# Kernel optimization log

Measured on AMD Instinct MI355X. Metric: run time of the kernel, lower is better.

The kernel has to match this reference:

```python
import jax, jax.numpy as jnp
import numpy as np

N, E, D, C, H = 50000, 800000, 128, 64, 2
NEG_SLOPE = 0.2


def gat_layer(x, src, dst, W, a_src, a_dst, b, heads, concat):
    # PyG GATConv (eval mode: attention dropout disabled), add_self_loops already in src/dst.
    n = x.shape[0]
    c = W.shape[1] // heads
    xl = (x @ W).reshape(n, heads, c)                      # [N,H,C]
    s = jnp.einsum('nhc,hc->nh', xl, a_src)                # alpha_src per node
    d = jnp.einsum('nhc,hc->nh', xl, a_dst)                # alpha_dst per node
    e = jax.nn.leaky_relu(s[src] + d[dst], NEG_SLOPE)      # [E,H]
    emax = jax.lax.stop_gradient(jax.ops.segment_max(e, dst, num_segments=n))
    ex = jnp.exp(e - emax[dst])
    denom = jax.ops.segment_sum(ex, dst, num_segments=n)   # every node has a self-loop -> denom > 0
    alpha = ex / denom[dst]                                # softmax over incoming edges
    msg = xl[src] * alpha[:, :, None]                      # [E,H,C]
    out = jax.ops.segment_sum(msg, dst, num_segments=n)    # [N,H,C]
    out = out.reshape(n, heads * c) if concat else out.mean(axis=1)
    return out + b


def setup_inputs() -> dict:
    key = jax.random.key(0)
    ks = jax.random.split(key, 16)
    x = jax.random.normal(ks[0], (N, D), dtype=jnp.float32)
    edge_index = jax.random.randint(ks[1], (2, E), 0, N, dtype=jnp.int64)
    def glorot(k, shape):
        fan = shape[0] + shape[-1]
        return jax.random.normal(k, shape, dtype=jnp.float32) * np.sqrt(2.0 / fan).astype(np.float32)
    # layer 0: D -> H*C (concat)
    W0 = glorot(ks[2], (D, H * C)); att_src0 = glorot(ks[3], (H, C)); att_dst0 = glorot(ks[4], (H, C)); b0 = jnp.zeros((H * C,), jnp.float32)
    # layer 1: H*C -> H*C (concat)
    W1 = glorot(ks[5], (H * C, H * C)); att_src1 = glorot(ks[6], (H, C)); att_dst1 = glorot(ks[7], (H, C)); b1 = jnp.zeros((H * C,), jnp.float32)
    # layer 2: H*C -> C (heads=1, concat=False)
    W2 = glorot(ks[8], (H * C, C)); att_src2 = glorot(ks[9], (1, C)); att_dst2 = glorot(ks[10], (1, C)); b2 = jnp.zeros((C,), jnp.float32)
    return dict(x=x, edge_index=edge_index,
                W0=W0, att_src0=att_src0, att_dst0=att_dst0, b0=b0,
                W1=W1, att_src1=att_src1, att_dst1=att_dst1, b1=b1,
                W2=W2, att_src2=att_src2, att_dst2=att_dst2, b2=b2)


def reference(x, edge_index, W0, att_src0, att_dst0, b0, W1, att_src1, att_dst1, b1, W2, att_src2, att_dst2, b2):
    n = x.shape[0]
    loops = jnp.arange(n, dtype=edge_index.dtype)
    src = jnp.concatenate([edge_index[0], loops])
    dst = jnp.concatenate([edge_index[1], loops])
    h = gat_layer(x, src, dst, W0, att_src0, att_dst0, b0, H, True)
    h = jax.nn.elu(h)
    h = gat_layer(h, src, dst, W1, att_src1, att_dst1, b1, H, True)
    h = jax.nn.elu(h)
    h = gat_layer(h, src, dst, W2, att_src2, att_dst2, b2, 1, False)
    return h
```

## Files before the change

### kernel.cpp

```cpp
#include <hip/hip_runtime.h>
#include <hip/hip_fp16.h>
#include <math.h>

#define NEG_SLOPE 0.2f

__device__ __forceinline__ float lrelu(float v) { return v > 0.0f ? v : NEG_SLOPE * v; }

typedef _Float16 half8 __attribute__((ext_vector_type(8)));
typedef float floatx4 __attribute__((ext_vector_type(4)));


__global__ __launch_bounds__(256) void count_win_k(const int* __restrict__ dst,
                                                   int* __restrict__ counts,
                                                   int e, int winSize) {
  const int win = blockIdx.x & 7;
  const int lo = win * winSize;
  const int hi = lo + winSize;
  const int base = (blockIdx.x >> 3) * 4096 + threadIdx.x;
  for (int t = 0; t < 16; ++t) {
    int i = base + t * 256;
    if (i < e) {
      int d = dst[i];
      if (d >= lo && d < hi) atomicAdd(&counts[d], 1);
    }
  }
}

__global__ __launch_bounds__(256) void block_sum_k(const int* __restrict__ counts,
                                                   int* __restrict__ blockSums, int n) {
  int i = blockIdx.x * 256 + threadIdx.x;
  int v = (i < n) ? counts[i] : 0;
  for (int o = 32; o > 0; o >>= 1) v += __shfl_xor(v, o);
  __shared__ int ws[4];
  if ((threadIdx.x & 63) == 0) ws[threadIdx.x >> 6] = v;
  __syncthreads();
  if (threadIdx.x == 0) blockSums[blockIdx.x] = ws[0] + ws[1] + ws[2] + ws[3];
}

__global__ __launch_bounds__(256) void scan_sums_k(int* __restrict__ blockSums, int nb,
                                                   int* __restrict__ total_out) {
  __shared__ int sh[256];
  const int tid = threadIdx.x;
  int run = 0;
  for (int base = 0; base < nb; base += 256) {
    int i = base + tid;
    int v = (i < nb) ? blockSums[i] : 0;
    sh[tid] = v;
    __syncthreads();
    for (int o = 1; o < 256; o <<= 1) {
      int t = (tid >= o) ? sh[tid - o] : 0;
      __syncthreads();
      sh[tid] += t;
      __syncthreads();
    }
    int chunkTotal = sh[255];
    if (i < nb) blockSums[i] = run + sh[tid] - v;
    __syncthreads();
    run += chunkTotal;
  }
  if (tid == 0) *total_out = run;
}

__global__ __launch_bounds__(256) void scan_apply_k(int* __restrict__ counts_cursor,
                                                    const int* __restrict__ blockOffs,
                                                    int* __restrict__ row_ptr, int n) {
  __shared__ int sh[256];
  const int tid = threadIdx.x;
  const int i = blockIdx.x * 256 + tid;
  int v = (i < n) ? counts_cursor[i] : 0;
  sh[tid] = v;
  __syncthreads();
  for (int o = 1; o < 256; o <<= 1) {
    int t = (tid >= o) ? sh[tid - o] : 0;
    __syncthreads();
    sh[tid] += t;
    __syncthreads();
  }
  if (i < n) {
    int excl = blockOffs[blockIdx.x] + sh[tid] - v;
    row_ptr[i] = excl;
    counts_cursor[i] = excl;
  }
}

__global__ __launch_bounds__(256) void scatter_win_k(const int* __restrict__ src,
                                                     const int* __restrict__ dst,
                                                     int* __restrict__ cursor,
                                                     int* __restrict__ csr,
                                                     int e, int winSize) {
  const int win = blockIdx.x & 7;
  const int lo = win * winSize;
  const int hi = lo + winSize;
  const int base = (blockIdx.x >> 3) * 4096 + threadIdx.x;
  for (int t = 0; t < 16; ++t) {
    int i = base + t * 256;
    if (i < e) {
      int d = dst[i];
      if (d >= lo && d < hi) {
        int pos = atomicAdd(&cursor[d], 1);
        csr[pos] = src[i];
      }
    }
  }
}


__global__ __launch_bounds__(256) void cvt_wt3_k(const float* __restrict__ W0,
                                                 const float* __restrict__ W1,
                                                 const float* __restrict__ W2,
                                                 __half* __restrict__ Wt0,
                                                 __half* __restrict__ Wt1,
                                                 __half* __restrict__ Wt2) {
  int i = blockIdx.x * 256 + threadIdx.x;
  if (i < 128 * 128) {
    int col = i >> 7, k = i & 127;
    Wt0[i] = __float2half(W0[k * 128 + col]);
    Wt1[i] = __float2half(W1[k * 128 + col]);
    if (col < 64) Wt2[(size_t)col * 128 + k] = __float2half(W2[k * 64 + col]);
  }
}


template<int M, int H_, bool IN_F32>
__global__ __launch_bounds__(256) void gemm_attn_mfma_k(const void* __restrict__ Xin,
                                                        const __half* __restrict__ Wt,
                                                        const float* __restrict__ a_src,
                                                        const float* __restrict__ a_dst,
                                                        __half* __restrict__ Yh,
                                                        float* __restrict__ sArr,
                                                        float* __restrict__ dArr, int n) {
  constexpr int CT = M / 16;
  constexpr int LP = 136;
  __shared__ _Float16 Xs[64 * LP];
  __shared__ _Float16 Ws[M * LP];
  const int tid = threadIdx.x;
  const int w = tid >> 6;
  const int lane = tid & 63;
  const int l15 = lane & 15;
  const int quad = lane >> 4;
  const int rb = blockIdx.x * 64;

  if (IN_F32) {
    const float* Xf = (const float*)Xin;
    for (int t = 0; t < 8; ++t) {
      int idx = tid + t * 256;
      int r = idx >> 5, c4 = idx & 31;
      float4 v = make_float4(0.f, 0.f, 0.f, 0.f);
      if (rb + r < n) v = *(const float4*)(Xf + (size_t)(rb + r) * 128 + c4 * 4);
      __half2 a = __floats2half2_rn(v.x, v.y);
      __half2 b = __floats2half2_rn(v.z, v.w);
      uint2 pk;
      pk.x = *(unsigned int*)&a;
      pk.y = *(unsigned int*)&b;
      *(uint2*)&Xs[r * LP + c4 * 4] = pk;
    }
  } else {
    const __half* Xh = (const __half*)Xin;
    for (int t = 0; t < 4; ++t) {
      int idx = tid + t * 256;
      int r = idx >> 4, c8 = idx & 15;
      uint4 v = make_uint4(0, 0, 0, 0);
      if (rb + r < n) v = *(const uint4*)(Xh + (size_t)(rb + r) * 128 + c8 * 8);
      *(uint4*)&Xs[r * LP + c8 * 8] = v;
    }
  }
  for (int t = 0; t < CT; ++t) {
    int idx = tid + t * 256;
    int r = idx >> 4, c8 = idx & 15;
    *(uint4*)&Ws[r * LP + c8 * 8] = *(const uint4*)(Wt + (size_t)r * 128 + c8 * 8);
  }
  __syncthreads();

  floatx4 acc[CT];
  for (int c = 0; c < CT; ++c)
    for (int j = 0; j < 4; ++j) acc[c][j] = 0.f;

  const int arow = w * 16 + l15;
  for (int kq = 0; kq < 4; ++kq) {
    half8 a = *(const half8*)&Xs[arow * LP + kq * 32 + quad * 8];
    for (int c = 0; c < CT; ++c) {
      half8 b = *(const half8*)&Ws[(c * 16 + l15) * LP + kq * 32 + quad * 8];
      acc[c] = __builtin_amdgcn_mfma_f32_16x16x32_f16(a, b, acc[c], 0, 0, 0);
    }
  }

  float as[CT], ad[CT];
  for (int c = 0; c < CT; ++c) {
    as[c] = a_src[c * 16 + l15];
    ad[c] = a_dst[c * 16 + l15];
  }

  for (int c = 0; c < CT; ++c) {
    for (int r = 0; r < 4; ++r) {
      int row = rb + w * 16 + quad * 4 + r;
      if (row < n) Yh[(size_t)row * M + c * 16 + l15] = __float2half(acc[c][r]);
    }
  }

  for (int r = 0; r < 4; ++r) {
    int row = rb + w * 16 + quad * 4 + r;
    float s0 = 0.f, d0 = 0.f, s1 = 0.f, d1 = 0.f;
    if (H_ == 2) {
      for (int c = 0; c < CT / 2; ++c) {
        s0 += acc[c][r] * as[c];
        d0 += acc[c][r] * ad[c];
      }
      for (int c = CT / 2; c < CT; ++c) {
        s1 += acc[c][r] * as[c];
        d1 += acc[c][r] * ad[c];
      }
    } else {
      for (int c = 0; c < CT; ++c) {
        s0 += acc[c][r] * as[c];
        d0 += acc[c][r] * ad[c];
      }
    }
    for (int o = 1; o < 16; o <<= 1) {
      s0 += __shfl_xor(s0, o);
      d0 += __shfl_xor(d0, o);
      if (H_ == 2) {
        s1 += __shfl_xor(s1, o);
        d1 += __shfl_xor(d1, o);
      }
    }
    if (l15 == 0 && row < n) {
      if (H_ == 2) {
        sArr[row * 2] = s0;
        sArr[row * 2 + 1] = s1;
        dArr[row * 2] = d0;
        dArr[row * 2 + 1] = d1;
      } else {
        sArr[row] = s0;
        dArr[row] = d0;
      }
    }
  }
}


#define IDX_CAP 1024

__global__ __launch_bounds__(256) void edge2h_k(const __half* __restrict__ xlh,
                                                const float* __restrict__ sArr,
                                                const float* __restrict__ dArr,
                                                const float* __restrict__ bias,
                                                const int* __restrict__ row_ptr,
                                                const int* __restrict__ csr,
                                                __half* __restrict__ outh, int n) {
  const int tid = threadIdx.x;
  const int wid = tid >> 6;
  const int lane = tid & 63;
  const int sub = lane >> 4;
  const int l16 = lane & 15;
  const int nodeBase = blockIdx.x * 16;

  __shared__ int rp[17];
  __shared__ int idxS[IDX_CAP];
  if (tid < 17) {
    int nn = nodeBase + tid;
    rp[tid] = row_ptr[nn < n ? nn : n];
  }
  __syncthreads();
  const int rowBeg = rp[0];
  int lim = rp[16] - rowBeg;
  if (lim > IDX_CAP) lim = IDX_CAP;
  for (int i = tid; i < lim; i += 256) idxS[i] = csr[rowBeg + i];
  __syncthreads();

  const int li = (wid << 2) + sub;
  const int node = nodeBase + li;
  if (node >= n) return;
  const int row = rp[li];
  const int deg = rp[li + 1] - row;
  const int head = l16 >> 3;
  const uint4* __restrict__ xq = (const uint4*)xlh;
  const float dnsel = dArr[node * 2 + head];

  float svS = sArr[node * 2 + head];
  uint4 pS = xq[(size_t)node * 16 + l16];

  float a0 = 0.f, a1 = 0.f, a2 = 0.f, a3 = 0.f;
  float a4 = 0.f, a5 = 0.f, a6 = 0.f, a7 = 0.f;
  float den = 0.f;

  auto body = [&](const int* __restrict__ ip) {
    int j = 0;
    for (; j + 4 <= deg; j += 4) {
      int idx[4];
      float sv[4];
      uint4 p[4];
#pragma unroll
      for (int t = 0; t < 4; ++t) idx[t] = ip[j + t];
#pragma unroll
      for (int t = 0; t < 4; ++t) sv[t] = sArr[idx[t] * 2 + head];
#pragma unroll
      for (int t = 0; t < 4; ++t) p[t] = xq[(size_t)idx[t] * 16 + l16];
#pragma unroll
      for (int t = 0; t < 4; ++t) {
        float w = __expf(lrelu(sv[t] + dnsel));
        den += w;
        float2 v0 = __half22float2(*(__half2*)&p[t].x);
        float2 v1 = __half22float2(*(__half2*)&p[t].y);
        float2 v2 = __half22float2(*(__half2*)&p[t].z);
        float2 v3 = __half22float2(*(__half2*)&p[t].w);
        a0 += w * v0.x; a1 += w * v0.y; a2 += w * v1.x; a3 += w * v1.y;
        a4 += w * v2.x; a5 += w * v2.y; a6 += w * v3.x; a7 += w * v3.y;
      }
    }
    for (; j < deg; ++j) {
      int i0 = ip[j];
      float sv = sArr[i0 * 2 + head];
      uint4 p = xq[(size_t)i0 * 16 + l16];
      float w = __expf(lrelu(sv + dnsel));
      den += w;
      float2 v0 = __half22float2(*(__half2*)&p.x);
      float2 v1 = __half22float2(*(__half2*)&p.y);
      float2 v2 = __half22float2(*(__half2*)&p.z);
      float2 v3 = __half22float2(*(__half2*)&p.w);
      a0 += w * v0.x; a1 += w * v0.y; a2 += w * v1.x; a3 += w * v1.y;
      a4 += w * v2.x; a5 += w * v2.y; a6 += w * v3.x; a7 += w * v3.y;
    }
  };
  if (row - rowBeg + deg <= IDX_CAP) body(idxS + (row - rowBeg));
  else body(csr + row);

  float wS = __expf(lrelu(svS + dnsel));
  den += wS;
  {
    float2 v0 = __half22float2(*(__half2*)&pS.x);
    float2 v1 = __half22float2(*(__half2*)&pS.y);
    float2 v2 = __half22float2(*(__half2*)&pS.z);
    float2 v3 = __half22float2(*(__half2*)&pS.w);
    a0 += wS * v0.x; a1 += wS * v0.y; a2 += wS * v1.x; a3 += wS * v1.y;
    a4 += wS * v2.x; a5 += wS * v2.y; a6 += wS * v3.x; a7 += wS * v3.y;
  }

  float wi = 1.f / den;
  float4 bbA = ((const float4*)bias)[l16 * 2];
  float4 bbB = ((const float4*)bias)[l16 * 2 + 1];
  float r0 = a0 * wi + bbA.x;
  float r1 = a1 * wi + bbA.y;
  float r2 = a2 * wi + bbA.z;
  float r3 = a3 * wi + bbA.w;
  float r4 = a4 * wi + bbB.x;
  float r5 = a5 * wi + bbB.y;
  float r6 = a6 * wi + bbB.z;
  float r7 = a7 * wi + bbB.w;
  r0 = r0 > 0.f ? r0 : expm1f(r0);
  r1 = r1 > 0.f ? r1 : expm1f(r1);
  r2 = r2 > 0.f ? r2 : expm1f(r2);
  r3 = r3 > 0.f ? r3 : expm1f(r3);
  r4 = r4 > 0.f ? r4 : expm1f(r4);
  r5 = r5 > 0.f ? r5 : expm1f(r5);
  r6 = r6 > 0.f ? r6 : expm1f(r6);
  r7 = r7 > 0.f ? r7 : expm1f(r7);
  __half2 h0 = __floats2half2_rn(r0, r1);
  __half2 h1 = __floats2half2_rn(r2, r3);
  __half2 h2 = __floats2half2_rn(r4, r5);
  __half2 h3 = __floats2half2_rn(r6, r7);
  uint4 pk;
  pk.x = *(unsigned int*)&h0;
  pk.y = *(unsigned int*)&h1;
  pk.z = *(unsigned int*)&h2;
  pk.w = *(unsigned int*)&h3;
  ((uint4*)outh)[(size_t)node * 16 + l16] = pk;
}

__global__ __launch_bounds__(256) void edge1h_k(const __half* __restrict__ xlh,
                                                const float* __restrict__ sArr,
                                                const float* __restrict__ dArr,
                                                const float* __restrict__ bias,
                                                const int* __restrict__ row_ptr,
                                                const int* __restrict__ csr,
                                                float* __restrict__ outp, int n) {
  const int tid = threadIdx.x;
  const int wid = tid >> 6;
  const int lane = tid & 63;
  const int sub = lane >> 4;
  const int l16 = lane & 15;
  const int nodeBase = blockIdx.x * 16;

  __shared__ int rp[17];
  __shared__ int idxS[IDX_CAP];
  if (tid < 17) {
    int nn = nodeBase + tid;
    rp[tid] = row_ptr[nn < n ? nn : n];
  }
  __syncthreads();
  const int rowBeg = rp[0];
  int lim = rp[16] - rowBeg;
  if (lim > IDX_CAP) lim = IDX_CAP;
  for (int i = tid; i < lim; i += 256) idxS[i] = csr[rowBeg + i];
  __syncthreads();

  const int li = (wid << 2) + sub;
  const int node = nodeBase + li;
  if (node >= n) return;
  const int row = rp[li];
  const int deg = rp[li + 1] - row;
  const uint2* __restrict__ xq = (const uint2*)xlh;
  const float dn = dArr[node];

  float svS = sArr[node];
  uint2 pS = xq[(size_t)node * 16 + l16];

  float a0 = 0.f, a1 = 0.f, a2 = 0.f, a3 = 0.f;
  float den = 0.f;

  auto body = [&](const int* __restrict__ ip) {
    int j = 0;
    for (; j + 4 <= deg; j += 4) {
      int idx[4];
      float sv[4];
      uint2 p[4];
#pragma unroll
      for (int t = 0; t < 4; ++t) idx[t] = ip[j + t];
#pragma unroll
      for (int t = 0; t < 4; ++t) sv[t] = sArr[idx[t]];
#pragma unroll
      for (int t = 0; t < 4; ++t) p[t] = xq[(size_t)idx[t] * 16 + l16];
#pragma unroll
      for (int t = 0; t < 4; ++t) {
        float w = __expf(lrelu(sv[t] + dn));
        den += w;
        float2 v0 = __half22float2(*(__half2*)&p[t].x);
        float2 v1 = __half22float2(*(__half2*)&p[t].y);
        a0 += w * v0.x; a1 += w * v0.y; a2 += w * v1.x; a3 += w * v1.y;
      }
    }
    for (; j < deg; ++j) {
      int i0 = ip[j];
      float sv = sArr[i0];
      uint2 p = xq[(size_t)i0 * 16 + l16];
      float w = __expf(lrelu(sv + dn));
      den += w;
      float2 v0 = __half22float2(*(__half2*)&p.x);
      float2 v1 = __half22float2(*(__half2*)&p.y);
      a0 += w * v0.x; a1 += w * v0.y; a2 += w * v1.x; a3 += w * v1.y;
    }
  };
  if (row - rowBeg + deg <= IDX_CAP) body(idxS + (row - rowBeg));
  else body(csr + row);

  float wS = __expf(lrelu(svS + dn));
  den += wS;
  {
    float2 v0 = __half22float2(*(__half2*)&pS.x);
    float2 v1 = __half22float2(*(__half2*)&pS.y);
    a0 += wS * v0.x; a1 += wS * v0.y; a2 += wS * v1.x; a3 += wS * v1.y;
  }

  float wi = 1.f / den;
  float4 bb = ((const float4*)bias)[l16];
  float4 r;
  r.x = a0 * wi + bb.x;
  r.y = a1 * wi + bb.y;
  r.z = a2 * wi + bb.z;
  r.w = a3 * wi + bb.w;
  ((float4*)outp)[(size_t)node * 16 + l16] = r;
}


extern "C" void kernel_launch(void* const* d_in, const int* in_sizes, int n_in,
                              void* d_out, int out_size, void* d_ws, size_t ws_size,
                              hipStream_t stream) {
  const float* x  = (const float*)d_in[0];
  const int* ei   = (const int*)d_in[1];
  const float* W0 = (const float*)d_in[2];
  const float* as0 = (const float*)d_in[3];
  const float* ad0 = (const float*)d_in[4];
  const float* b0 = (const float*)d_in[5];
  const float* W1 = (const float*)d_in[6];
  const float* as1 = (const float*)d_in[7];
  const float* ad1 = (const float*)d_in[8];
  const float* b1 = (const float*)d_in[9];
  const float* W2 = (const float*)d_in[10];
  const float* as2 = (const float*)d_in[11];
  const float* ad2 = (const float*)d_in[12];
  const float* b2 = (const float*)d_in[13];
  float* out = (float*)d_out;

  const int n = in_sizes[0] / 128;
  const int e = in_sizes[1] / 2;
  const int* srcIdx = ei;
  const int* dstIdx = ei + e;

  float* ws = (float*)d_ws;
  float* sArr = ws;
  float* dArr = sArr + (size_t)n * 2;
  __half* xlh = (__half*)(dArr + (size_t)n * 2);
  __half* bufHh = xlh + (size_t)n * 128;
  __half* Wt0 = bufHh + (size_t)n * 128;
  __half* Wt1 = Wt0 + 128 * 128;
  __half* Wt2 = Wt1 + 128 * 128;
  int* csr = (int*)(Wt2 + 64 * 128);
  int* row_ptr = csr + e;
  int* cursor = row_ptr + (n + 1);
  int* blockSums = cursor + n;

  const int nb = (n + 255) / 256;
  const int winSize = (n + 7) / 8;
  const int gwin = 8 * ((e + 4095) / 4096);

  cvt_wt3_k<<<(128 * 128 + 255) / 256, 256, 0, stream>>>(W0, W1, W2, Wt0, Wt1, Wt2);

  hipMemsetAsync(cursor, 0, (size_t)n * sizeof(int), stream);
  count_win_k<<<gwin, 256, 0, stream>>>(dstIdx, cursor, e, winSize);
  block_sum_k<<<nb, 256, 0, stream>>>(cursor, blockSums, n);
  scan_sums_k<<<1, 256, 0, stream>>>(blockSums, nb, row_ptr + n);
  scan_apply_k<<<nb, 256, 0, stream>>>(cursor, blockSums, row_ptr, n);
  scatter_win_k<<<gwin, 256, 0, stream>>>(srcIdx, dstIdx, cursor, csr, e, winSize);

  const int gb = (n + 63) / 64;
  const int gq = (n + 15) / 16;

  gemm_attn_mfma_k<128, 2, true><<<gb, 256, 0, stream>>>(x, Wt0, as0, ad0, xlh, sArr, dArr, n);
  edge2h_k<<<gq, 256, 0, stream>>>(xlh, sArr, dArr, b0, row_ptr, csr, bufHh, n);

  gemm_attn_mfma_k<128, 2, false><<<gb, 256, 0, stream>>>(bufHh, Wt1, as1, ad1, xlh, sArr, dArr, n);
  edge2h_k<<<gq, 256, 0, stream>>>(xlh, sArr, dArr, b1, row_ptr, csr, bufHh, n);

  gemm_attn_mfma_k<64, 1, false><<<gb, 256, 0, stream>>>(bufHh, Wt2, as2, ad2, xlh, sArr, dArr, n);
  edge1h_k<<<gq, 256, 0, stream>>>(xlh, sArr, dArr, b2, row_ptr, csr, out, n);
}
```

Baseline: 302.0 us.

## Fuse CSR count and prefix scan into one kernel with grid-wide spin barriers

```diff
diff --git a/kernel.cpp b/kernel.cpp
--- a/kernel.cpp
+++ b/kernel.cpp
@@ -3,6 +3,7 @@
 #include <math.h>
 
 #define NEG_SLOPE 0.2f
+#define IDX_CAP 1024
 
 __device__ __forceinline__ float lrelu(float v) { return v > 0.0f ? v : NEG_SLOPE * v; }
 
@@ -10,64 +11,65 @@
 typedef float floatx4 __attribute__((ext_vector_type(4)));
 
 
-__global__ __launch_bounds__(256) void count_win_k(const int* __restrict__ dst,
-                                                   int* __restrict__ counts,
-                                                   int e, int winSize) {
-  const int win = blockIdx.x & 7;
-  const int lo = win * winSize;
-  const int hi = lo + winSize;
-  const int base = (blockIdx.x >> 3) * 4096 + threadIdx.x;
-  for (int t = 0; t < 16; ++t) {
-    int i = base + t * 256;
-    if (i < e) {
-      int d = dst[i];
-      if (d >= lo && d < hi) atomicAdd(&counts[d], 1);
-    }
-  }
-}
-
-__global__ __launch_bounds__(256) void block_sum_k(const int* __restrict__ counts,
-                                                   int* __restrict__ blockSums, int n) {
-  int i = blockIdx.x * 256 + threadIdx.x;
-  int v = (i < n) ? counts[i] : 0;
-  for (int o = 32; o > 0; o >>= 1) v += __shfl_xor(v, o);
-  __shared__ int ws[4];
-  if ((threadIdx.x & 63) == 0) ws[threadIdx.x >> 6] = v;
-  __syncthreads();
-  if (threadIdx.x == 0) blockSums[blockIdx.x] = ws[0] + ws[1] + ws[2] + ws[3];
-}
-
-__global__ __launch_bounds__(256) void scan_sums_k(int* __restrict__ blockSums, int nb,
-                                                   int* __restrict__ total_out) {
+__global__ __launch_bounds__(256) void cvt_wt3_zero_k(const float* __restrict__ W0,
+                                                      const float* __restrict__ W1,
+                                                      const float* __restrict__ W2,
+                                                      __half* __restrict__ Wt0,
+                                                      __half* __restrict__ Wt1,
+                                                      __half* __restrict__ Wt2,
+                                                      int* __restrict__ cursor,
+                                                      int* __restrict__ ctl, int n) {
+  const int i = blockIdx.x * 256 + threadIdx.x;
+  const int stride = gridDim.x * 256;
+  for (int k = i; k < n; k += stride) cursor[k] = 0;
+  if (blockIdx.x == 0 && threadIdx.x < 4) ctl[threadIdx.x] = 0;
+  if (i < 128 * 128) {
+    int col = i >> 7, k = i & 127;
+    Wt0[i] = __float2half(W0[k * 128 + col]);
+    Wt1[i] = __float2half(W1[k * 128 + col]);
+    if (col < 64) Wt2[(size_t)col * 128 + k] = __float2half(W2[k * 64 + col]);
+  }
+}
+
+
+__global__ __launch_bounds__(256) void count_scan_k(const int* __restrict__ dst,
+                                                    int* __restrict__ cursor,
+                                                    int* __restrict__ row_ptr,
+                                                    int* __restrict__ blockSums,
+                                                    int* __restrict__ ctl,
+                                                    int n, int e, int winSize, int nbc) {
+  const int tid = threadIdx.x;
+
+  {
+    const int win = blockIdx.x & 7;
+    const int lo = win * winSize;
+    const int hi = lo + winSize;
+    const int base = (blockIdx.x >> 3) * 4096 + tid;
+    for (int t = 0; t < 16; ++t) {
+      int i = base + t * 256;
+      if (i < e) {
+        int d = dst[i];
+        if (d >= lo && d < hi) atomicAdd(&cursor[d], 1);
+      }
+    }
+  }
+  __threadfence();
+  if (tid == 0)
+    __hip_atomic_fetch_add(&ctl[0], 1, __ATOMIC_ACQ_REL, __HIP_MEMORY_SCOPE_AGENT);
+  if (blockIdx.x >= nbc) return;
+
+  if (tid == 0) {
+    while (__hip_atomic_load(&ctl[0], __ATOMIC_ACQUIRE, __HIP_MEMORY_SCOPE_AGENT) <
+           (int)gridDim.x)
+      __builtin_amdgcn_s_sleep(2);
+  }
+  __syncthreads();
+
   __shared__ int sh[256];
-  const int tid = threadIdx.x;
-  int run = 0;
-  for (int base = 0; base < nb; base += 256) {
-    int i = base + tid;
-    int v = (i < nb) ? blockSums[i] : 0;
-    sh[tid] = v;
-    __syncthreads();
-    for (int o = 1; o < 256; o <<= 1) {
-      int t = (tid >= o) ? sh[tid - o] : 0;
-      __syncthreads();
-      sh[tid] += t;
-      __syncthreads();
-    }
-    int chunkTotal = sh[255];
-    if (i < nb) blockSums[i] = run + sh[tid] - v;
-    __syncthreads();
-    run += chunkTotal;
-  }
-  if (tid == 0) *total_out = run;
-}
-
-__global__ __launch_bounds__(256) void scan_apply_k(int* __restrict__ counts_cursor,
-                                                    const int* __restrict__ blockOffs,
-                                                    int* __restrict__ row_ptr, int n) {
-  __shared__ int sh[256];
-  const int tid = threadIdx.x;
-  const int i = blockIdx.x * 256 + tid;
-  int v = (i < n) ? counts_cursor[i] : 0;
+  __shared__ int shTicket;
+  const int chunk = blockIdx.x;
+  const int gi = chunk * 256 + tid;
+  int v = (gi < n) ? cursor[gi] : 0;
   sh[tid] = v;
   __syncthreads();
   for (int o = 1; o < 256; o <<= 1) {
@@ -76,12 +78,52 @@
     sh[tid] += t;
     __syncthreads();
   }
-  if (i < n) {
-    int excl = blockOffs[blockIdx.x] + sh[tid] - v;
-    row_ptr[i] = excl;
-    counts_cursor[i] = excl;
-  }
-}
+  const int excl = sh[tid] - v;
+  const int total = sh[255];
+  if (tid == 0) blockSums[chunk] = total;
+  __threadfence();
+  if (tid == 0)
+    shTicket = __hip_atomic_fetch_add(&ctl[1], 1, __ATOMIC_ACQ_REL,
+                                      __HIP_MEMORY_SCOPE_AGENT);
+  __syncthreads();
+
+  if (shTicket == nbc - 1) {
+    int run = 0;
+    for (int base = 0; base < nbc; base += 256) {
+      int j = base + tid;
+      int bv = (j < nbc) ? blockSums[j] : 0;
+      __syncthreads();
+      sh[tid] = bv;
+      __syncthreads();
+      for (int o = 1; o < 256; o <<= 1) {
+        int t = (tid >= o) ? sh[tid - o] : 0;
+        __syncthreads();
+        sh[tid] += t;
+        __syncthreads();
+      }
+      int ct = sh[255];
+      if (j < nbc) blockSums[j] = run + sh[tid] - bv;
+      __syncthreads();
+      run += ct;
+    }
+    if (tid == 0) row_ptr[n] = run;
+    __threadfence();
+    if (tid == 0)
+      __hip_atomic_store(&ctl[2], 1, __ATOMIC_RELEASE, __HIP_MEMORY_SCOPE_AGENT);
+  }
+
+  if (tid == 0) {
+    while (__hip_atomic_load(&ctl[2], __ATOMIC_ACQUIRE, __HIP_MEMORY_SCOPE_AGENT) == 0)
+      __builtin_amdgcn_s_sleep(2);
+  }
+  __syncthreads();
+  if (gi < n) {
+    int ex = blockSums[chunk] + excl;
+    row_ptr[gi] = ex;
+    cursor[gi] = ex;
+  }
+}
+
 
 __global__ __launch_bounds__(256) void scatter_win_k(const int* __restrict__ src,
                                                      const int* __restrict__ dst,
@@ -101,22 +143,6 @@
         csr[pos] = src[i];
       }
     }
-  }
-}
-
-
-__global__ __launch_bounds__(256) void cvt_wt3_k(const float* __restrict__ W0,
-                                                 const float* __restrict__ W1,
-                                                 const float* __restrict__ W2,
-                                                 __half* __restrict__ Wt0,
-                                                 __half* __restrict__ Wt1,
-                                                 __half* __restrict__ Wt2) {
-  int i = blockIdx.x * 256 + threadIdx.x;
-  if (i < 128 * 128) {
-    int col = i >> 7, k = i & 127;
-    Wt0[i] = __float2half(W0[k * 128 + col]);
-    Wt1[i] = __float2half(W1[k * 128 + col]);
-    if (col < 64) Wt2[(size_t)col * 128 + k] = __float2half(W2[k * 64 + col]);
   }
 }
 
@@ -237,8 +263,6 @@
   }
 }
 
-
-#define IDX_CAP 1024
 
 __global__ __launch_bounds__(256) void edge2h_k(const __half* __restrict__ xlh,
                                                 const float* __restrict__ sArr,
@@ -497,18 +521,15 @@
   int* row_ptr = csr + e;
   int* cursor = row_ptr + (n + 1);
   int* blockSums = cursor + n;
-
   const int nb = (n + 255) / 256;
+  int* ctl = blockSums + nb;
+
   const int winSize = (n + 7) / 8;
   const int gwin = 8 * ((e + 4095) / 4096);
 
-  cvt_wt3_k<<<(128 * 128 + 255) / 256, 256, 0, stream>>>(W0, W1, W2, Wt0, Wt1, Wt2);
-
-  hipMemsetAsync(cursor, 0, (size_t)n * sizeof(int), stream);
-  count_win_k<<<gwin, 256, 0, stream>>>(dstIdx, cursor, e, winSize);
-  block_sum_k<<<nb, 256, 0, stream>>>(cursor, blockSums, n);
-  scan_sums_k<<<1, 256, 0, stream>>>(blockSums, nb, row_ptr + n);
-  scan_apply_k<<<nb, 256, 0, stream>>>(cursor, blockSums, row_ptr, n);
+  cvt_wt3_zero_k<<<nb, 256, 0, stream>>>(W0, W1, W2, Wt0, Wt1, Wt2, cursor, ctl, n);
+  count_scan_k<<<gwin, 256, 0, stream>>>(dstIdx, cursor, row_ptr, blockSums, ctl,
+                                         n, e, winSize, nb);
   scatter_win_k<<<gwin, 256, 0, stream>>>(srcIdx, dstIdx, cursor, csr, e, winSize);
 
   const int gb = (n + 63) / 64;
```

New measurement: 468.6 us. +55.2%, slower.
